# Kernel tuning notes

Measured on AMD Instinct MI355X. Metric: run time of the kernel, lower is better.

The kernel has to match this reference:

```python
import jax, jax.numpy as jnp
import numpy as np

NHEAD = 8
LN_EPS = 1e-5


def _layernorm(x, g, b):
    mu = jnp.mean(x, -1, keepdims=True)
    var = jnp.mean((x - mu) ** 2, -1, keepdims=True)
    return (x - mu) / jnp.sqrt(var + LN_EPS) * g + b


def _sparse_attn(q, k, v, P):
    # Topology: P queries attend to P keys; G queries attend to P keys + self.
    # q,k,v: [B,H,L,dh], keys/values restricted to pcpt block [B,H,P,dh]
    dh = q.shape[-1]
    scale = 1.0 / jnp.sqrt(jnp.asarray(dh, q.dtype))
    kp, vp = k[:, :, :P], v[:, :, :P]
    S = jnp.einsum('bhld,bhpd->bhlp', q, kp) * scale  # [B,H,L,P]
    # pcpt queries: plain softmax over P keys
    out_p = jnp.einsum('bhqp,bhpd->bhqd', jax.nn.softmax(S[:, :, :P], axis=-1), vp)
    # gen queries: P keys + own diagonal key
    qg, kg, vg = q[:, :, P:], k[:, :, P:], v[:, :, P:]
    Sg = S[:, :, P:]                                   # [B,H,G,P]
    dlog = jnp.sum(qg * kg, -1) * scale                # [B,H,G] diagonal logits
    m = jnp.maximum(jnp.max(Sg, -1), dlog)
    eg = jnp.exp(Sg - m[..., None])
    ed = jnp.exp(dlog - m)
    den = jnp.sum(eg, -1) + ed
    out_g = (jnp.einsum('bhgp,bhpd->bhgd', eg, vp) + ed[..., None] * vg) / den[..., None]
    return jnp.concatenate([out_p, out_g], axis=2)     # [B,H,L,dh]


def _forward(pcpt, gen, Wqkv, bqkv, Wo, bo, W1, b1, W2, b2, g1, beta1, g2, beta2):
    P = pcpt.shape[1]
    x = jnp.concatenate([pcpt, gen], axis=1)           # [B,L,d]
    B, L, d = x.shape
    dh = d // NHEAD
    for i in range(Wqkv.shape[0]):  # post-norm layers
        qkv = (x @ Wqkv[i] + bqkv[i]).reshape(B, L, 3, NHEAD, dh)
        q = jnp.transpose(qkv[:, :, 0], (0, 2, 1, 3))
        k = jnp.transpose(qkv[:, :, 1], (0, 2, 1, 3))
        v = jnp.transpose(qkv[:, :, 2], (0, 2, 1, 3))
        a = _sparse_attn(q, k, v, P)
        a = jnp.transpose(a, (0, 2, 1, 3)).reshape(B, L, d)
        a = a @ Wo[i] + bo[i]
        x = _layernorm(x + a, g1[i], beta1[i])
        h = jax.nn.relu(x @ W1[i] + b1[i]) @ W2[i] + b2[i]
        x = _layernorm(x + h, g2[i], beta2[i])
    return x


def setup_inputs() -> dict:
    key = jax.random.key(0)
    ks = jax.random.split(key, 16)
    B, P, G, d, ff, Lyr = 4, 1024, 1024, 512, 2048, 4
    s = 0.02
    f32 = jnp.float32
    return {
        'pcpt_total_embs': jax.random.normal(ks[0], (B, P, d), f32),
        'gen_total_embs': jax.random.normal(ks[1], (B, G, d), f32),
        'src_key_padding_mask': jnp.zeros((B, P + G), bool),
        'Wqkv': jax.random.normal(ks[2], (Lyr, d, 3 * d), f32) * s,
        'bqkv': jnp.zeros((Lyr, 3 * d), f32),
        'Wo': jax.random.normal(ks[3], (Lyr, d, d), f32) * s,
        'bo': jnp.zeros((Lyr, d), f32),
        'W1': jax.random.normal(ks[4], (Lyr, d, ff), f32) * s,
        'b1': jnp.zeros((Lyr, ff), f32),
        'W2': jax.random.normal(ks[5], (Lyr, ff, d), f32) * s,
        'b2': jnp.zeros((Lyr, d), f32),
        'g1': jnp.ones((Lyr, d), f32),
        'beta1': jnp.zeros((Lyr, d), f32),
        'g2': jnp.ones((Lyr, d), f32),
        'beta2': jnp.zeros((Lyr, d), f32),
    }


def reference(pcpt_total_embs, gen_total_embs, src_key_padding_mask, Wqkv, bqkv, Wo, bo, W1, b1, W2, b2, g1, beta1, g2, beta2):
    P = pcpt_total_embs.shape[1]
    x = _forward(pcpt_total_embs, gen_total_embs, Wqkv, bqkv, Wo, bo, W1, b1, W2, b2, g1, beta1, g2, beta2)
    return x[:, :P], x[:, P:]
```

## Files before the change

### kernel.cpp

```cpp
#include <hip/hip_runtime.h>
#include <hip/hip_bf16.h>

#define B_ 4
#define P_ 1024
#define G_ 1024
#define L_ 2048
#define D_ 512
#define FF_ 2048
#define H_ 8
#define DH_ 64
#define LAYERS_ 4
#define LN_EPS_ 1e-5f

typedef __attribute__((ext_vector_type(8))) short bf16x8;
typedef __attribute__((ext_vector_type(4))) float f32x4;

__device__ __forceinline__ ushort f2b(float f) {
  unsigned u = __float_as_uint(f);
  unsigned r = (u + 0x7fffu + ((u >> 16) & 1u)) >> 16;
  return (ushort)r;
}
__device__ __forceinline__ float b2f(ushort u) {
  return __uint_as_float(((unsigned)u) << 16);
}

__device__ __forceinline__ void gld16(const ushort* g, ushort* l) {
  __builtin_amdgcn_global_load_lds(
      (const __attribute__((address_space(1))) void*)g,
      (__attribute__((address_space(3))) void*)l, 16, 0, 0);
}

__global__ __launch_bounds__(256) void concat_kernel(const float* __restrict__ p,
    const float* __restrict__ g, float* __restrict__ x, ushort* __restrict__ xb)
{
  const int LD4 = L_*D_/4, PD4 = P_*D_/4;
  int i = blockIdx.x*256 + threadIdx.x;
  int b = i / LD4, r = i - b*LD4;
  float4 v;
  if (r < PD4) v = ((const float4*)p)[(size_t)b*PD4 + r];
  else         v = ((const float4*)g)[(size_t)b*PD4 + (r-PD4)];
  ((float4*)x)[i] = v;
  ushort4 h; h.x=f2b(v.x); h.y=f2b(v.y); h.z=f2b(v.z); h.w=f2b(v.w);
  ((ushort4*)xb)[i] = h;
}

__global__ __launch_bounds__(256) void writeout_kernel(const float* __restrict__ x,
    float* __restrict__ out)
{
  const int LD4 = L_*D_/4, PD4 = P_*D_/4, HALF = B_*PD4;
  int i = blockIdx.x*256 + threadIdx.x;
  int half = (i >= HALF) ? 1 : 0;
  int r = i - half*HALF;
  int b = r / PD4, q = r - b*PD4;
  ((float4*)out)[i] = ((const float4*)x)[(size_t)b*LD4 + half*PD4 + q];
}

__global__ __launch_bounds__(256) void wconv_kernel(const float* __restrict__ src,
    ushort* __restrict__ dst, int K, int N)
{
  __shared__ float tile[32][33];
  int n0 = blockIdx.x*32, k0 = blockIdx.y*32, l = blockIdx.z;
  src += (size_t)l*K*N; dst += (size_t)l*K*N;
  int tx = threadIdx.x & 31, ty = threadIdx.x >> 5;
  #pragma unroll
  for (int u=0;u<4;++u) tile[ty+8*u][tx] = src[(size_t)(k0+ty+8*u)*N + n0+tx];
  __syncthreads();
  #pragma unroll
  for (int u=0;u<4;++u) dst[(size_t)(n0+ty+8*u)*K + k0+tx] = f2b(tile[tx][ty+8*u]);
}

template<int BN_, int RELU, int RES, int OUTBF>
__global__ __launch_bounds__(256) void mgemm(
    const ushort* __restrict__ A, const ushort* __restrict__ Bt,
    const float* __restrict__ bias, const float* __restrict__ res,
    void* __restrict__ Cout, int M, int N, int K)
{
  constexpr int MI = (BN_ == 128) ? 4 : 2;
  constexpr int BL = BN_ / 32;
  __shared__ ushort As[2*128*64];
  __shared__ ushort Bs[2*BN_*64];
  int t = threadIdx.x;
  int lane = t & 63, w = t >> 6;
  int wm = (BN_ == 128) ? (w >> 1) * 64 : w * 32;
  int wn = (BN_ == 128) ? (w & 1) * 64 : 0;
  int m0 = blockIdx.x * 128, n0 = blockIdx.y * BN_;

  f32x4 acc[MI][4] = {};

  int rbase = t >> 3;
  int cch   = (t & 7) ^ ((t >> 3) & 7);
  const ushort* Ag = A  + (size_t)(m0 + rbase)*K + cch*8;
  const ushort* Bg = Bt + (size_t)(n0 + rbase)*K + cch*8;
  ushort* Asl0 = As + t*8;
  ushort* Asl1 = As + 128*64 + t*8;
  ushort* Bsl0 = Bs + t*8;
  ushort* Bsl1 = Bs + BN_*64 + t*8;
  const size_t rowK32 = (size_t)32 * K;

  int fr = lane & 15, fq = lane >> 4;
  int swr[2];
  swr[0] = ((0*4 + fq) ^ (fr & 7)) * 8;
  swr[1] = ((1*4 + fq) ^ (fr & 7)) * 8;

  #pragma unroll
  for (int L = 0; L < 4; ++L)  gld16(Ag + L*rowK32, Asl0 + L*2048);
  #pragma unroll
  for (int L = 0; L < BL; ++L) gld16(Bg + L*rowK32, Bsl0 + L*2048);

  const int NT = K >> 6;
  for (int tt = 0; tt < NT; ++tt) {
    asm volatile("s_waitcnt vmcnt(0)" ::: "memory");
    __builtin_amdgcn_s_barrier();
    __builtin_amdgcn_sched_barrier(0);
    if (tt + 1 < NT) {
      const ushort* Agn = Ag + (size_t)(tt+1)*64;
      const ushort* Bgn = Bg + (size_t)(tt+1)*64;
      ushort* Ad = (tt & 1) ? Asl0 : Asl1;
      ushort* Bd = (tt & 1) ? Bsl0 : Bsl1;
      #pragma unroll
      for (int L = 0; L < 4; ++L)  gld16(Agn + L*rowK32, Ad + L*2048);
      #pragma unroll
      for (int L = 0; L < BL; ++L) gld16(Bgn + L*rowK32, Bd + L*2048);
    }
    const ushort* Ard = ((tt & 1) ? As + 128*64 : As) + (wm + fr)*64;
    const ushort* Brd = ((tt & 1) ? Bs + BN_*64 : Bs) + (wn + fr)*64;
    #pragma unroll
    for (int s = 0; s < 2; ++s) {
      int sw = swr[s];
      bf16x8 af[MI], bfr[4];
      #pragma unroll
      for (int i=0;i<MI;++i) af[i]  = *(const bf16x8*)(Ard + i*16*64 + sw);
      #pragma unroll
      for (int j=0;j<4;++j)  bfr[j] = *(const bf16x8*)(Brd + j*16*64 + sw);
      #pragma unroll
      for (int i=0;i<MI;++i)
        #pragma unroll
        for (int j=0;j<4;++j)
          acc[i][j] = __builtin_amdgcn_mfma_f32_16x16x32_bf16(af[i], bfr[j], acc[i][j], 0, 0, 0);
    }
  }

  int ncol = lane & 15;
  int rquad = (lane >> 4) * 4;
  #pragma unroll
  for (int j=0;j<4;++j) {
    int n = n0 + wn + j*16 + ncol;
    float bv = bias[n];
    #pragma unroll
    for (int i=0;i<MI;++i) {
      int mbase = m0 + wm + i*16 + rquad;
      #pragma unroll
      for (int r=0;r<4;++r) {
        int m = mbase + r;
        float c = acc[i][j][r] + bv;
        if (RES) c += res[(size_t)m*N + n];
        if (RELU) c = fmaxf(c, 0.f);
        if (OUTBF) ((ushort*)Cout)[(size_t)m*N + n] = f2b(c);
        else       ((float*)Cout)[(size_t)m*N + n] = c;
      }
    }
  }
}

__global__ __launch_bounds__(256) void mgemm_qkv(
    const ushort* __restrict__ A,
    const ushort* __restrict__ Bt,
    const float* __restrict__ bias,
    ushort* __restrict__ qb,
    ushort* __restrict__ kb,
    ushort* __restrict__ vtb)
{
  const int K = D_;
  __shared__ ushort As[2*128*64];
  __shared__ ushort Bs[2*128*64];
  int t = threadIdx.x;
  int lane = t & 63, w = t >> 6;
  int wm = (w >> 1) * 64, wn = (w & 1) * 64;
  int m0 = blockIdx.x * 128, n0 = blockIdx.y * 128;

  f32x4 acc[4][4] = {};

  int rbase = t >> 3;
  int cch   = (t & 7) ^ ((t >> 3) & 7);
  const ushort* Ag = A  + (size_t)(m0 + rbase)*K + cch*8;
  const ushort* Bg = Bt + (size_t)(n0 + rbase)*K + cch*8;
  ushort* Asl0 = As + t*8;
  ushort* Asl1 = As + 128*64 + t*8;
  ushort* Bsl0 = Bs + t*8;
  ushort* Bsl1 = Bs + 128*64 + t*8;
  const size_t rowK32 = (size_t)32 * K;

  int fr = lane & 15, fq = lane >> 4;
  int swr[2];
  swr[0] = ((0*4 + fq) ^ (fr & 7)) * 8;
  swr[1] = ((1*4 + fq) ^ (fr & 7)) * 8;

  #pragma unroll
  for (int L = 0; L < 4; ++L) gld16(Ag + L*rowK32, Asl0 + L*2048);
  #pragma unroll
  for (int L = 0; L < 4; ++L) gld16(Bg + L*rowK32, Bsl0 + L*2048);

  const int NT = K >> 6;
  for (int tt = 0; tt < NT; ++tt) {
    asm volatile("s_waitcnt vmcnt(0)" ::: "memory");
    __builtin_amdgcn_s_barrier();
    __builtin_amdgcn_sched_barrier(0);
    if (tt + 1 < NT) {
      const ushort* Agn = Ag + (size_t)(tt+1)*64;
      const ushort* Bgn = Bg + (size_t)(tt+1)*64;
      ushort* Ad = (tt & 1) ? Asl0 : Asl1;
      ushort* Bd = (tt & 1) ? Bsl0 : Bsl1;
      #pragma unroll
      for (int L = 0; L < 4; ++L) gld16(Agn + L*rowK32, Ad + L*2048);
      #pragma unroll
      for (int L = 0; L < 4; ++L) gld16(Bgn + L*rowK32, Bd + L*2048);
    }
    const ushort* Ard = ((tt & 1) ? As + 128*64 : As) + (wm + fr)*64;
    const ushort* Brd = ((tt & 1) ? Bs + 128*64 : Bs) + (wn + fr)*64;
    #pragma unroll
    for (int s = 0; s < 2; ++s) {
      int sw = swr[s];
      bf16x8 af[4], bfr[4];
      #pragma unroll
      for (int i=0;i<4;++i) af[i]  = *(const bf16x8*)(Ard + i*16*64 + sw);
      #pragma unroll
      for (int j=0;j<4;++j) bfr[j] = *(const bf16x8*)(Brd + j*16*64 + sw);
      #pragma unroll
      for (int i=0;i<4;++i)
        #pragma unroll
        for (int j=0;j<4;++j)
          acc[i][j] = __builtin_amdgcn_mfma_f32_16x16x32_bf16(af[i], bfr[j], acc[i][j], 0, 0, 0);
    }
  }

  int ncol = lane & 15;
  int rquad = (lane >> 4) * 4;
  #pragma unroll
  for (int j=0;j<4;++j) {
    int n = n0 + wn + j*16 + ncol;
    float bv = bias[n];
    int part = n >> 9;
    int wi = n & 511;
    int h = wi >> 6, d = wi & 63;
    #pragma unroll
    for (int i=0;i<4;++i) {
      int mbase = m0 + wm + i*16 + rquad;
      #pragma unroll
      for (int r=0;r<4;++r) {
        int m = mbase + r;
        int b = m >> 11, l = m & 2047;
        int bh = b*H_ + h;
        float cv = acc[i][j][r] + bv;
        if (part == 0) cv *= 0.125f;
        ushort c = f2b(cv);
        if (part == 0)      qb[((size_t)bh*L_ + l)*DH_ + d] = c;
        else if (part == 1) kb[((size_t)bh*L_ + l)*DH_ + d] = c;
        else                vtb[((size_t)bh*DH_ + d)*L_ + l] = c;
      }
    }
  }
}

__global__ __launch_bounds__(256) void attn_mfma(
    const ushort* __restrict__ qb, const ushort* __restrict__ kb,
    const ushort* __restrict__ vtb, ushort* __restrict__ outa)
{
  __shared__ ushort Ks[2][64*64];
  __shared__ ushort Vts[2][64*64];
  __shared__ ushort Ps[8*16*72];

  int t = threadIdx.x;
  int lane = t & 63, w = t >> 6;
  int qt = blockIdx.x & 15;
  int h  = (blockIdx.x >> 4) & 7;
  int b  = blockIdx.x >> 7;
  int l0 = qt * 128;
  bool isgen = (l0 >= P_);
  int bh = b*H_ + h;

  const ushort* qg  = qb  + ((size_t)bh*L_ + l0)*DH_;
  const ushort* kgb = kb  + (size_t)bh*L_*DH_;
  const ushort* vtg = vtb + (size_t)bh*DH_*L_;

  int sr  = t >> 3;
  int scg = (t & 7) * 8;
  int scs = ((t & 7) ^ (sr & 7)) * 8;

  int fr = lane & 15, fq = lane >> 4;
  int swz0 = ((0*4 + fq) ^ (fr & 7)) * 8;
  int swz1 = ((1*4 + fq) ^ (fr & 7)) * 8;

  bf16x8 qf[2][2];
  #pragma unroll
  for (int i=0;i<2;++i) {
    qf[i][0] = *(const bf16x8*)(qg + (size_t)(w*32 + i*16 + fr)*DH_ + fq*8);
    qf[i][1] = *(const bf16x8*)(qg + (size_t)(w*32 + i*16 + fr)*DH_ + 32 + fq*8);
  }

  float den[2][4] = {};
  f32x4 o[2][4] = {};
  ushort* Pw0 = Ps + (w*2 + 0)*16*72;
  ushort* Pw1 = Ps + (w*2 + 1)*16*72;

  {
    uint4 a0 = *(const uint4*)(kgb + (size_t)sr*DH_ + scg);
    uint4 a1 = *(const uint4*)(kgb + (size_t)(sr+32)*DH_ + scg);
    uint4 a2 = *(const uint4*)(vtg + (size_t)sr*L_ + scg);
    uint4 a3 = *(const uint4*)(vtg + (size_t)(sr+32)*L_ + scg);
    *(uint4*)(&Ks[0][sr*64 + scs])       = a0;
    *(uint4*)(&Ks[0][(sr+32)*64 + scs])  = a1;
    *(uint4*)(&Vts[0][sr*64 + scs])      = a2;
    *(uint4*)(&Vts[0][(sr+32)*64 + scs]) = a3;
  }
  uint4 pk0 = *(const uint4*)(kgb + (size_t)(64+sr)*DH_ + scg);
  uint4 pk1 = *(const uint4*)(kgb + (size_t)(64+sr+32)*DH_ + scg);
  uint4 pv0 = *(const uint4*)(vtg + (size_t)sr*L_ + 64 + scg);
  uint4 pv1 = *(const uint4*)(vtg + (size_t)(sr+32)*L_ + 64 + scg);
  __syncthreads();

  for (int kt = 0; kt < 16; ++kt) {
    const ushort* Kc = &Ks[kt & 1][0];
    const ushort* Vc = &Vts[kt & 1][0];
    if (kt < 15) {
      ushort* Kn = &Ks[(kt+1) & 1][0];
      ushort* Vn = &Vts[(kt+1) & 1][0];
      *(uint4*)(Kn + sr*64 + scs)      = pk0;
      *(uint4*)(Kn + (sr+32)*64 + scs) = pk1;
      *(uint4*)(Vn + sr*64 + scs)      = pv0;
      *(uint4*)(Vn + (sr+32)*64 + scs) = pv1;
    }
    if (kt < 14) {
      int p2 = (kt + 2) * 64;
      pk0 = *(const uint4*)(kgb + (size_t)(p2+sr)*DH_ + scg);
      pk1 = *(const uint4*)(kgb + (size_t)(p2+sr+32)*DH_ + scg);
      pv0 = *(const uint4*)(vtg + (size_t)sr*L_ + p2 + scg);
      pv1 = *(const uint4*)(vtg + (size_t)(sr+32)*L_ + p2 + scg);
    }

    f32x4 sc4[2][4] = {};
    __builtin_amdgcn_s_setprio(1);
    #pragma unroll
    for (int s=0;s<2;++s) {
      int sw = s ? swz1 : swz0;
      #pragma unroll
      for (int j=0;j<4;++j) {
        bf16x8 kf = *(const bf16x8*)(Kc + (j*16 + fr)*64 + sw);
        sc4[0][j] = __builtin_amdgcn_mfma_f32_16x16x32_bf16(qf[0][s], kf, sc4[0][j], 0, 0, 0);
        sc4[1][j] = __builtin_amdgcn_mfma_f32_16x16x32_bf16(qf[1][s], kf, sc4[1][j], 0, 0, 0);
      }
    }
    __builtin_amdgcn_s_setprio(0);

    #pragma unroll
    for (int i=0;i<2;++i) {
      ushort* Pw = i ? Pw1 : Pw0;
      #pragma unroll
      for (int r=0;r<4;++r) {
        float e0 = __expf(sc4[i][0][r]);
        float e1 = __expf(sc4[i][1][r]);
        float e2 = __expf(sc4[i][2][r]);
        float e3 = __expf(sc4[i][3][r]);
        den[i][r] += (e0+e1) + (e2+e3);
        Pw[(fq*4+r)*72 +  0 + fr] = (ushort)(__float_as_uint(e0) >> 16);
        Pw[(fq*4+r)*72 + 16 + fr] = (ushort)(__float_as_uint(e1) >> 16);
        Pw[(fq*4+r)*72 + 32 + fr] = (ushort)(__float_as_uint(e2) >> 16);
        Pw[(fq*4+r)*72 + 48 + fr] = (ushort)(__float_as_uint(e3) >> 16);
      }
    }
    asm volatile("s_waitcnt lgkmcnt(0)" ::: "memory");

    __builtin_amdgcn_s_setprio(1);
    #pragma unroll
    for (int s=0;s<2;++s) {
      int sw = s ? swz1 : swz0;
      bf16x8 pf0 = *(const bf16x8*)(Pw0 + fr*72 + s*32 + fq*8);
      bf16x8 pf1 = *(const bf16x8*)(Pw1 + fr*72 + s*32 + fq*8);
      #pragma unroll
      for (int j=0;j<4;++j) {
        bf16x8 vf = *(const bf16x8*)(Vc + (j*16 + fr)*64 + sw);
        o[0][j] = __builtin_amdgcn_mfma_f32_16x16x32_bf16(pf0, vf, o[0][j], 0, 0, 0);
        o[1][j] = __builtin_amdgcn_mfma_f32_16x16x32_bf16(pf1, vf, o[1][j], 0, 0, 0);
      }
    }
    __builtin_amdgcn_s_setprio(0);
    __syncthreads();
  }

  #pragma unroll
  for (int i=0;i<2;++i)
    #pragma unroll
    for (int r=0;r<4;++r) {
      float d = den[i][r];
      d += __shfl_xor(d, 1, 16);
      d += __shfl_xor(d, 2, 16);
      d += __shfl_xor(d, 4, 16);
      d += __shfl_xor(d, 8, 16);
      den[i][r] = d;
    }

  if (isgen) {
    #pragma unroll
    for (int i=0;i<2;++i) {
      int base = l0 + w*32 + i*16;
      f32x4 dsc = {};
      {
        bf16x8 kd0 = *(const bf16x8*)(kgb + (size_t)(base + fr)*DH_ + fq*8);
        dsc = __builtin_amdgcn_mfma_f32_16x16x32_bf16(qf[i][0], kd0, dsc, 0, 0, 0);
        bf16x8 kd1 = *(const bf16x8*)(kgb + (size_t)(base + fr)*DH_ + 32 + fq*8);
        dsc = __builtin_amdgcn_mfma_f32_16x16x32_bf16(qf[i][1], kd1, dsc, 0, 0, 0);
      }
      #pragma unroll
      for (int r=0;r<4;++r) {
        int m = fq*4 + r;
        float dl = __shfl(dsc[r], fq*16 + m);
        float ed = __expf(dl);
        den[i][r] += ed;
        int l = base + m;
        #pragma unroll
        for (int j=0;j<4;++j) {
          float vv = b2f(vtg[(size_t)(j*16 + fr)*L_ + l]);
          o[i][j][r] += ed*vv;
        }
      }
    }
  }

  #pragma unroll
  for (int i=0;i<2;++i)
    #pragma unroll
    for (int r=0;r<4;++r) {
      float inv = 1.f / den[i][r];
      int l = l0 + w*32 + i*16 + fq*4 + r;
      #pragma unroll
      for (int j=0;j<4;++j)
        outa[((size_t)b*L_ + l)*D_ + h*DH_ + j*16 + fr] = f2b(o[i][j][r]*inv);
    }
}

__global__ __launch_bounds__(64) void ln_kernel(const float* __restrict__ y,
    const float* __restrict__ gw, const float* __restrict__ bw,
    float* __restrict__ x, ushort* __restrict__ xb)
{
  int row = blockIdx.x, t = threadIdx.x;
  const float4* yr = (const float4*)(y + (size_t)row*D_);
  float4 v0 = yr[t], v1 = yr[t+64];
  float s = v0.x+v0.y+v0.z+v0.w + v1.x+v1.y+v1.z+v1.w;
  for (int off=32; off>0; off>>=1) s += __shfl_down(s, off, 64);
  s = __shfl(s, 0, 64);
  float mu = s * (1.f/D_);
  float dx;
  float q = 0.f;
  dx=v0.x-mu; q+=dx*dx; dx=v0.y-mu; q+=dx*dx; dx=v0.z-mu; q+=dx*dx; dx=v0.w-mu; q+=dx*dx;
  dx=v1.x-mu; q+=dx*dx; dx=v1.y-mu; q+=dx*dx; dx=v1.z-mu; q+=dx*dx; dx=v1.w-mu; q+=dx*dx;
  for (int off=32; off>0; off>>=1) q += __shfl_down(q, off, 64);
  q = __shfl(q, 0, 64);
  float rinv = rsqrtf(q*(1.f/D_) + LN_EPS_);
  const float4* g4 = (const float4*)gw;
  const float4* b4 = (const float4*)bw;
  float4 gv0=g4[t], gv1=g4[t+64], bv0=b4[t], bv1=b4[t+64];
  float4 o0, o1;
  o0.x=(v0.x-mu)*rinv*gv0.x+bv0.x; o0.y=(v0.y-mu)*rinv*gv0.y+bv0.y;
  o0.z=(v0.z-mu)*rinv*gv0.z+bv0.z; o0.w=(v0.w-mu)*rinv*gv0.w+bv0.w;
  o1.x=(v1.x-mu)*rinv*gv1.x+bv1.x; o1.y=(v1.y-mu)*rinv*gv1.y+bv1.y;
  o1.z=(v1.z-mu)*rinv*gv1.z+bv1.z; o1.w=(v1.w-mu)*rinv*gv1.w+bv1.w;
  float4* xr = (float4*)(x + (size_t)row*D_);
  xr[t]=o0; xr[t+64]=o1;
  ushort4 h0, h1;
  h0.x=f2b(o0.x); h0.y=f2b(o0.y); h0.z=f2b(o0.z); h0.w=f2b(o0.w);
  h1.x=f2b(o1.x); h1.y=f2b(o1.y); h1.z=f2b(o1.z); h1.w=f2b(o1.w);
  ushort4* xbr = (ushort4*)(xb + (size_t)row*D_);
  xbr[t]=h0; xbr[t+64]=h1;
}

extern "C" void kernel_launch(void* const* d_in, const int* in_sizes, int n_in,
                              void* d_out, int out_size, void* d_ws, size_t ws_size,
                              hipStream_t stream) {
  const float* pcpt = (const float*)d_in[0];
  const float* gen  = (const float*)d_in[1];
  const float* Wqkv = (const float*)d_in[3];
  const float* bqkv = (const float*)d_in[4];
  const float* Wo   = (const float*)d_in[5];
  const float* bo   = (const float*)d_in[6];
  const float* W1   = (const float*)d_in[7];
  const float* b1   = (const float*)d_in[8];
  const float* W2   = (const float*)d_in[9];
  const float* b2   = (const float*)d_in[10];
  const float* g1   = (const float*)d_in[11];
  const float* be1  = (const float*)d_in[12];
  const float* g2   = (const float*)d_in[13];
  const float* be2  = (const float*)d_in[14];
  float* out = (float*)d_out;

  const size_t XD  = (size_t)B_*L_*D_;
  const size_t HKV = (size_t)B_*H_*L_*DH_;
  const size_t HFF = (size_t)B_*L_*FF_;

  float*  xbuf = (float*)d_ws;
  ushort* xbf  = (ushort*)(xbuf + XD);
  ushort* region = xbf + XD;
  ushort* qb  = region;
  ushort* kb  = region + HKV;
  ushort* vtb = region + 2*HKV;
  ushort* hbf = region;
  ushort* abf = region + HFF;
  ushort* wb  = abf + XD;
  ushort* wqkv_b = wb;
  ushort* wo_b   = wqkv_b + (size_t)4*3*D_*D_;
  ushort* w1_b   = wo_b   + (size_t)4*D_*D_;
  ushort* w2_b   = w1_b   + (size_t)4*FF_*D_;
  float*  ybuf = out;

  const int M = B_*L_;

  wconv_kernel<<<dim3(3*D_/32, D_/32, 4), 256, 0, stream>>>(Wqkv, wqkv_b, D_, 3*D_);
  wconv_kernel<<<dim3(D_/32,   D_/32, 4), 256, 0, stream>>>(Wo,   wo_b,   D_, D_);
  wconv_kernel<<<dim3(FF_/32,  D_/32, 4), 256, 0, stream>>>(W1,   w1_b,   D_, FF_);
  wconv_kernel<<<dim3(D_/32,  FF_/32, 4), 256, 0, stream>>>(W2,   w2_b,   FF_, D_);

  concat_kernel<<<4096, 256, 0, stream>>>(pcpt, gen, xbuf, xbf);

  for (int i = 0; i < LAYERS_; ++i) {
    const ushort* wqkv_i = wqkv_b + (size_t)i*3*D_*D_;
    const ushort* wo_i   = wo_b   + (size_t)i*D_*D_;
    const ushort* w1_i   = w1_b   + (size_t)i*FF_*D_;
    const ushort* w2_i   = w2_b   + (size_t)i*D_*FF_;
    const float* bqkv_i = bqkv + (size_t)i*3*D_;
    const float* bo_i   = bo   + (size_t)i*D_;
    const float* b1_i   = b1   + (size_t)i*FF_;
    const float* b2_i   = b2   + (size_t)i*D_;
    const float* g1_i   = g1   + (size_t)i*D_;
    const float* be1_i  = be1  + (size_t)i*D_;
    const float* g2_i   = g2   + (size_t)i*D_;
    const float* be2_i  = be2  + (size_t)i*D_;

    mgemm_qkv<<<dim3(M/128, 3*D_/128), 256, 0, stream>>>(
        xbf, wqkv_i, bqkv_i, qb, kb, vtb);

    attn_mfma<<<B_*H_*(L_/128), 256, 0, stream>>>(qb, kb, vtb, abf);

    mgemm<64,0,1,0><<<dim3(M/128, D_/64), 256, 0, stream>>>(
        abf, wo_i, bo_i, xbuf, ybuf, M, D_, D_);

    ln_kernel<<<M, 64, 0, stream>>>(ybuf, g1_i, be1_i, xbuf, xbf);

    mgemm<128,1,0,1><<<dim3(M/128, FF_/128), 256, 0, stream>>>(
        xbf, w1_i, b1_i, nullptr, hbf, M, FF_, D_);

    mgemm<64,0,1,0><<<dim3(M/128, D_/64), 256, 0, stream>>>(
        hbf, w2_i, b2_i, xbuf, ybuf, M, D_, FF_);

    ln_kernel<<<M, 64, 0, stream>>>(ybuf, g2_i, be2_i, xbuf, xbf);
  }

  writeout_kernel<<<4096, 256, 0, stream>>>(xbuf, out);
}
```

Before: 782.7 us.

## Replace double-buffered LDS pipeline in mgemm with single-buffer load-then-compute loop

```diff
diff --git a/kernel.cpp b/kernel.cpp
--- a/kernel.cpp
+++ b/kernel.cpp
@@ -77,8 +77,8 @@
 {
   constexpr int MI = (BN_ == 128) ? 4 : 2;
   constexpr int BL = BN_ / 32;
-  __shared__ ushort As[2*128*64];
-  __shared__ ushort Bs[2*BN_*64];
+  __shared__ ushort As[128*64];
+  __shared__ ushort Bs[BN_*64];
   int t = threadIdx.x;
   int lane = t & 63, w = t >> 6;
   int wm = (BN_ == 128) ? (w >> 1) * 64 : w * 32;
@@ -91,39 +91,25 @@
   int cch   = (t & 7) ^ ((t >> 3) & 7);
   const ushort* Ag = A  + (size_t)(m0 + rbase)*K + cch*8;
   const ushort* Bg = Bt + (size_t)(n0 + rbase)*K + cch*8;
-  ushort* Asl0 = As + t*8;
-  ushort* Asl1 = As + 128*64 + t*8;
-  ushort* Bsl0 = Bs + t*8;
-  ushort* Bsl1 = Bs + BN_*64 + t*8;
+  ushort* Asl = As + t*8;
+  ushort* Bsl = Bs + t*8;
   const size_t rowK32 = (size_t)32 * K;
 
   int fr = lane & 15, fq = lane >> 4;
   int swr[2];
   swr[0] = ((0*4 + fq) ^ (fr & 7)) * 8;
   swr[1] = ((1*4 + fq) ^ (fr & 7)) * 8;
-
-  #pragma unroll
-  for (int L = 0; L < 4; ++L)  gld16(Ag + L*rowK32, Asl0 + L*2048);
-  #pragma unroll
-  for (int L = 0; L < BL; ++L) gld16(Bg + L*rowK32, Bsl0 + L*2048);
-
-  const int NT = K >> 6;
-  for (int tt = 0; tt < NT; ++tt) {
-    asm volatile("s_waitcnt vmcnt(0)" ::: "memory");
-    __builtin_amdgcn_s_barrier();
-    __builtin_amdgcn_sched_barrier(0);
-    if (tt + 1 < NT) {
-      const ushort* Agn = Ag + (size_t)(tt+1)*64;
-      const ushort* Bgn = Bg + (size_t)(tt+1)*64;
-      ushort* Ad = (tt & 1) ? Asl0 : Asl1;
-      ushort* Bd = (tt & 1) ? Bsl0 : Bsl1;
-      #pragma unroll
-      for (int L = 0; L < 4; ++L)  gld16(Agn + L*rowK32, Ad + L*2048);
-      #pragma unroll
-      for (int L = 0; L < BL; ++L) gld16(Bgn + L*rowK32, Bd + L*2048);
-    }
-    const ushort* Ard = ((tt & 1) ? As + 128*64 : As) + (wm + fr)*64;
-    const ushort* Brd = ((tt & 1) ? Bs + BN_*64 : Bs) + (wn + fr)*64;
+  const ushort* Ard = As + (wm + fr)*64;
+  const ushort* Brd = Bs + (wn + fr)*64;
+
+  for (int k0 = 0; k0 < K; k0 += 64) {
+    __syncthreads();
+    #pragma unroll
+    for (int L = 0; L < 4; ++L)  gld16(Ag + L*rowK32, Asl + L*2048);
+    #pragma unroll
+    for (int L = 0; L < BL; ++L) gld16(Bg + L*rowK32, Bsl + L*2048);
+    Ag += 64; Bg += 64;
+    __syncthreads();
     #pragma unroll
     for (int s = 0; s < 2; ++s) {
       int sw = swr[s];
```

Result: no change. 788.0 us (+0.7%).
